# Optimization experiments

Measured on AMD Instinct MI355X. Metric: run time of the kernel, lower is better.

Reference implementation:

```python
import jax, jax.numpy as jnp
import numpy as np

N_NODES = 100000
N_EDGES = 1600000
IN_CH = 128
OUT_CH = 128


def setup_inputs() -> dict:
    key = jax.random.key(0)
    k1, k2, k3 = jax.random.split(key, 3)
    x = jax.random.normal(k1, (N_NODES, IN_CH), dtype=jnp.float32)
    edge_index = jax.random.randint(k2, (2, N_EDGES), 0, N_NODES, dtype=jnp.int64)
    # glorot-like init for the linear weight, stored as [in, out]
    W = jax.random.normal(k3, (IN_CH, OUT_CH), dtype=jnp.float32) * (2.0 / (IN_CH + OUT_CH)) ** 0.5
    bias = jnp.zeros((OUT_CH,), dtype=jnp.float32)
    return {"x": x, "edge_index": edge_index, "W": W, "bias": bias}


def reference(x, edge_index, W, bias):
    N = x.shape[0]
    # linear transform (bias-free, matches Linear(in, out, bias=False))
    h = x @ W  # [N, out]

    # add self loops (improved=False -> fill_value = 1.0)
    loop = jnp.arange(N, dtype=edge_index.dtype)
    src = jnp.concatenate([edge_index[0], loop])
    dst = jnp.concatenate([edge_index[1], loop])
    ew = jnp.ones(src.shape[0], dtype=h.dtype)  # edge_weight None -> ones

    # symmetric GCN normalization: deg from dst, norm = d^-1/2[src] * w * d^-1/2[dst]
    deg = jax.ops.segment_sum(ew, dst, num_segments=N)
    deg_inv_sqrt = jnp.where(deg > 0, jax.lax.rsqrt(deg), 0.0)
    w = deg_inv_sqrt[src] * ew * deg_inv_sqrt[dst]

    # spmm aggregation: out[dst] += w * h[src]
    out = jax.ops.segment_sum(h[src] * w[:, None], dst, num_segments=N)
    return out + bias
```

## Files before the change

### kernel.cpp

```cpp
#include <hip/hip_runtime.h>
#include <hip/hip_bf16.h>

constexpr int kNodes = 100000;
constexpr int kEdges = 1600000;
constexpr int kCh    = 128;
constexpr int kCap   = 32;
constexpr int kOvfCap = 8192;
constexpr int kPartSize = kNodes / 8;
constexpr int kCntStride = 32;
constexpr int kFillBlocks = 512;
constexpr int kGemmBlocks = (kNodes + 127) / 128;

typedef __attribute__((ext_vector_type(8))) short short8;
typedef __attribute__((ext_vector_type(4))) float floatx4;
typedef __attribute__((ext_vector_type(4))) int   intx4;


__global__ __launch_bounds__(512) void k_fused(const float* __restrict__ x,
                                               const float* __restrict__ W,
                                               const int* __restrict__ srcArr,
                                               const int* __restrict__ dstArr,
                                               int* __restrict__ cntPad,
                                               int* __restrict__ bucket,
                                               int* __restrict__ ovfCnt,
                                               int* __restrict__ ovfD,
                                               int* __restrict__ ovfS,
                                               __hip_bfloat16* __restrict__ hs) {
  if (blockIdx.x < kFillBlocks) {
    int part = blockIdx.x & 7;
    int bip  = blockIdx.x >> 3;
    int lo = part * kPartSize;
    const intx4* d4 = (const intx4*)dstArr;
    const intx4* s4 = (const intx4*)srcArr;
    for (int i = bip * 512 + (int)threadIdx.x; i < kEdges / 4; i += (kFillBlocks >> 3) * 512) {
      intx4 dv = __builtin_nontemporal_load(d4 + i);
      intx4 sv = __builtin_nontemporal_load(s4 + i);
      #pragma unroll
      for (int k = 0; k < 4; k++) {
        int d = dv[k];
        if ((unsigned)(d - lo) < (unsigned)kPartSize) {
          int pos = atomicAdd(&cntPad[(long)d * kCntStride], 1);
          if (pos < kCap) {
            bucket[(long)d * kCap + pos] = sv[k];
          } else {
            int o = atomicAdd(ovfCnt, 1);
            if (o < kOvfCap) { ovfD[o] = d; ovfS[o] = sv[k]; }
          }
        }
      }
    }
    return;
  }

  __shared__ short8 Bf[2048];
  for (int e = threadIdx.x; e < 2048; e += 512) {
    int lane = e & 63, c = (e >> 6) & 3, tt = e >> 8;
    int quad = lane >> 4, mcol = lane & 15;
    short8 v;
    #pragma unroll
    for (int j = 0; j < 8; j++) {
      __hip_bfloat16 h = __float2bfloat16(W[(c * 32 + quad * 8 + j) * kCh + tt * 16 + mcol]);
      v[j] = *(short*)&h;
    }
    Bf[e] = v;
  }
  __syncthreads();

  int wave = threadIdx.x >> 6;
  int lane = threadIdx.x & 63;
  int quad = lane >> 4;
  int mcol = lane & 15;
  int gb = blockIdx.x - kFillBlocks;
  long rowBase = ((long)gb * 8 + wave) * 16;
  if (rowBase >= kNodes) return;

  long arow = rowBase + mcol;
  if (arow >= kNodes) arow = kNodes - 1;
  const float* xp = x + arow * kCh;
  short8 afrag[4];
  #pragma unroll
  for (int c = 0; c < 4; c++) {
    const floatx4* p = (const floatx4*)(xp + c * 32 + quad * 8);
    floatx4 v0 = __builtin_nontemporal_load(p);
    floatx4 v1 = __builtin_nontemporal_load(p + 1);
    #pragma unroll
    for (int j = 0; j < 4; j++) {
      __hip_bfloat16 h0 = __float2bfloat16(v0[j]);
      __hip_bfloat16 h1 = __float2bfloat16(v1[j]);
      afrag[c][j]     = *(short*)&h0;
      afrag[c][j + 4] = *(short*)&h1;
    }
  }

  #pragma unroll
  for (int t = 0; t < 8; t++) {
    floatx4 acc = {0.f, 0.f, 0.f, 0.f};
    #pragma unroll
    for (int c = 0; c < 4; c++) {
      short8 b = Bf[(t * 4 + c) * 64 + lane];
      acc = __builtin_amdgcn_mfma_f32_16x16x32_bf16(afrag[c], b, acc, 0, 0, 0);
    }
    #pragma unroll
    for (int i = 0; i < 4; i++) {
      long r = rowBase + quad * 4 + i;
      if (r < kNodes) {
        __hip_bfloat16 h = __float2bfloat16(acc[i]);
        __builtin_nontemporal_store(*(short*)&h, (short*)hs + r * kCh + t * 16 + mcol);
      }
    }
  }
}


__global__ __launch_bounds__(256) void k_dinv(const int* __restrict__ cntPad,
                                              int* __restrict__ cntC,
                                              float* __restrict__ dinv) {
  int i = blockIdx.x * 256 + threadIdx.x;
  if (i < kNodes) {
    int c = cntPad[(long)i * kCntStride];
    cntC[i] = c;
    dinv[i] = rsqrtf((float)(c + 1));
  }
}


__global__ __launch_bounds__(256) void k_aggregate(const int* __restrict__ cntC,
                                                   const int* __restrict__ bucket,
                                                   const float* __restrict__ dinv,
                                                   const int* __restrict__ ovfCnt,
                                                   const int* __restrict__ ovfD,
                                                   const int* __restrict__ ovfS,
                                                   const __hip_bfloat16* __restrict__ hs,
                                                   const float* __restrict__ bias,
                                                   float* __restrict__ out) {
  int gid  = blockIdx.x * 256 + threadIdx.x;
  int node = gid >> 6;
  int lane = gid & 63;
  if (node >= kNodes) return;

  const __hip_bfloat162* hbase = (const __hip_bfloat162*)hs;

  int degRaw = cntC[node];
  float dd = dinv[node];

  float2 sf = __bfloat1622float2(hbase[(long)node * (kCh / 2) + lane]);
  float acc0 = dd * sf.x;
  float acc1 = dd * sf.y;

  int c = degRaw < kCap ? degRaw : kCap;
  const int* bkt = bucket + (long)node * kCap;

  int j = 0;
  for (; j + 7 < c; j += 8) {
    int s[8];
    #pragma unroll
    for (int u = 0; u < 8; u++) s[u] = bkt[j + u];
    float dv[8];
    #pragma unroll
    for (int u = 0; u < 8; u++) dv[u] = dinv[s[u]];
    __hip_bfloat162 v[8];
    #pragma unroll
    for (int u = 0; u < 8; u++) v[u] = hbase[(long)s[u] * (kCh / 2) + lane];
    #pragma unroll
    for (int u = 0; u < 8; u++) {
      float2 f = __bfloat1622float2(v[u]);
      acc0 = fmaf(dv[u], f.x, acc0);
      acc1 = fmaf(dv[u], f.y, acc1);
    }
  }
  for (; j < c; ++j) {
    int s = bkt[j];
    float dv = dinv[s];
    float2 f = __bfloat1622float2(hbase[(long)s * (kCh / 2) + lane]);
    acc0 = fmaf(dv, f.x, acc0);
    acc1 = fmaf(dv, f.y, acc1);
  }

  if (degRaw > kCap) {
    int n = *ovfCnt;
    if (n > kOvfCap) n = kOvfCap;
    for (int i = 0; i < n; i++) {
      if (ovfD[i] == node) {
        int s = ovfS[i];
        float2 f = __bfloat1622float2(hbase[(long)s * (kCh / 2) + lane]);
        acc0 = fmaf(dinv[s], f.x, acc0);
        acc1 = fmaf(dinv[s], f.y, acc1);
      }
    }
  }

  float2 b = ((const float2*)bias)[lane];
  float2 o;
  o.x = dd * acc0 + b.x;
  o.y = dd * acc1 + b.y;
  ((float2*)(out + (long)node * kCh))[lane] = o;
}


extern "C" void kernel_launch(void* const* d_in, const int* in_sizes, int n_in,
                              void* d_out, int out_size, void* d_ws, size_t ws_size,
                              hipStream_t stream) {
  const float* x    = (const float*)d_in[0];
  const int*   ei   = (const int*)d_in[1];
  const float* W    = (const float*)d_in[2];
  const float* bias = (const float*)d_in[3];
  float* out = (float*)d_out;

  const int* srcArr = ei;
  const int* dstArr = ei + kEdges;

  char* ws = (char*)d_ws;
  size_t off = 0;
  __hip_bfloat16* hs = (__hip_bfloat16*)(ws + off); off += (size_t)kNodes * kCh * 2;
  int*   bucket  = (int*)  (ws + off); off += (size_t)kNodes * kCap * 4;
  float* dinv    = (float*)(ws + off); off += (size_t)kNodes * 4;
  int*   cntC    = (int*)  (ws + off); off += (size_t)kNodes * 4;
  char* zbase = ws + off;
  int*   cntPad  = (int*)  (ws + off); off += (size_t)kNodes * kCntStride * 4;
  int*   ovfCnt  = (int*)  (ws + off); off += 128;
  size_t zbytes = (size_t)((ws + off) - zbase);
  int*   ovfD    = (int*)(ws + off); off += (size_t)kOvfCap * 4;
  int*   ovfS    = (int*)(ws + off); off += (size_t)kOvfCap * 4;

  (void)hipMemsetAsync(zbase, 0, zbytes, stream);

  k_fused<<<kFillBlocks + kGemmBlocks, 512, 0, stream>>>(x, W, srcArr, dstArr, cntPad, bucket,
                                                         ovfCnt, ovfD, ovfS, hs);

  k_dinv<<<(kNodes + 255) / 256, 256, 0, stream>>>(cntPad, cntC, dinv);

  long aggThreads = (long)kNodes * 64;
  int gAgg = (int)((aggThreads + 255) / 256);
  k_aggregate<<<gAgg, 256, 0, stream>>>(cntC, bucket, dinv, ovfCnt, ovfD, ovfS,
                                        hs, bias, out);
}
```

Before: 272.4 us.

## Replace global-atomic bucket fill with two-pass LDS binning of edges

The edge bucketing now runs in two passes. In the first, 128 blocks bin edges by destination range into per-block, per-bin chunks, packing dst offset and src into one word and counting with LDS atomics. In the second, a new fill kernel gathers each bin's chunks, builds the per-node buckets in shared memory, writes them out coalesced, and computes dinv. This replaces the scattered global atomics on padded counters and the separate dinv kernel. The cost is an extra intermediate buffer, chunk-overflow handling through a global flag that sends every node into the overflow scan, and a serial loop over 128 chunks per fill block.

After: 303.0 us. +11.2%, slower.

```diff
diff --git a/kernel.cpp b/kernel.cpp
--- a/kernel.cpp
+++ b/kernel.cpp
@@ -5,11 +5,15 @@
 constexpr int kEdges = 1600000;
 constexpr int kCh    = 128;
 constexpr int kCap   = 32;
-constexpr int kOvfCap = 8192;
-constexpr int kPartSize = kNodes / 8;
-constexpr int kCntStride = 32;
-constexpr int kFillBlocks = 512;
+constexpr int kOvfCap = 4096;
+constexpr int kBinShift = 11;
+constexpr int kBinSize  = 1 << kBinShift;
+constexpr int kBins  = (kNodes + kBinSize - 1) >> kBinShift;
+constexpr int kBinBlocks = 128;
+constexpr int kChunkCap = 384;
 constexpr int kGemmBlocks = (kNodes + 127) / 128;
+constexpr int kNodesPerB = 512;
+constexpr int kFillBlocks = (kNodes + kNodesPerB - 1) / kNodesPerB;
 
 typedef __attribute__((ext_vector_type(8))) short short8;
 typedef __attribute__((ext_vector_type(4))) float floatx4;
@@ -20,34 +24,43 @@
                                                const float* __restrict__ W,
                                                const int* __restrict__ srcArr,
                                                const int* __restrict__ dstArr,
-                                               int* __restrict__ cntPad,
-                                               int* __restrict__ bucket,
+                                               unsigned* __restrict__ segs,
+                                               int* __restrict__ segCnt,
+                                               int* __restrict__ cntA,
                                                int* __restrict__ ovfCnt,
+                                               int* __restrict__ ovfAFlag,
                                                int* __restrict__ ovfD,
                                                int* __restrict__ ovfS,
                                                __hip_bfloat16* __restrict__ hs) {
-  if (blockIdx.x < kFillBlocks) {
-    int part = blockIdx.x & 7;
-    int bip  = blockIdx.x >> 3;
-    int lo = part * kPartSize;
+  __shared__ int lcnt[kBins];
+  if (blockIdx.x < kBinBlocks) {
+    for (int i = threadIdx.x; i < kBins; i += 512) lcnt[i] = 0;
+    __syncthreads();
     const intx4* d4 = (const intx4*)dstArr;
     const intx4* s4 = (const intx4*)srcArr;
-    for (int i = bip * 512 + (int)threadIdx.x; i < kEdges / 4; i += (kFillBlocks >> 3) * 512) {
+    unsigned* myseg = segs + (long)blockIdx.x * kBins * kChunkCap;
+    for (int i = blockIdx.x * 512 + (int)threadIdx.x; i < kEdges / 4; i += kBinBlocks * 512) {
       intx4 dv = __builtin_nontemporal_load(d4 + i);
       intx4 sv = __builtin_nontemporal_load(s4 + i);
       #pragma unroll
       for (int k = 0; k < 4; k++) {
-        int d = dv[k];
-        if ((unsigned)(d - lo) < (unsigned)kPartSize) {
-          int pos = atomicAdd(&cntPad[(long)d * kCntStride], 1);
-          if (pos < kCap) {
-            bucket[(long)d * kCap + pos] = sv[k];
-          } else {
-            int o = atomicAdd(ovfCnt, 1);
-            if (o < kOvfCap) { ovfD[o] = d; ovfS[o] = sv[k]; }
-          }
+        int d = dv[k], s = sv[k];
+        int bin = d >> kBinShift;
+        int pos = atomicAdd(&lcnt[bin], 1);
+        if (pos < kChunkCap) {
+          myseg[bin * kChunkCap + pos] = ((unsigned)(d & (kBinSize - 1)) << 17) | (unsigned)s;
+        } else {
+          int o = atomicAdd(ovfCnt, 1);
+          if (o < kOvfCap) { ovfD[o] = d; ovfS[o] = s; }
+          atomicAdd(&cntA[d], 1);
+          atomicAdd(ovfAFlag, 1);
         }
       }
+    }
+    __syncthreads();
+    for (int i = threadIdx.x; i < kBins; i += 512) {
+      int c = lcnt[i];
+      segCnt[blockIdx.x * kBins + i] = c < kChunkCap ? c : kChunkCap;
     }
     return;
   }
@@ -70,7 +83,7 @@
   int lane = threadIdx.x & 63;
   int quad = lane >> 4;
   int mcol = lane & 15;
-  int gb = blockIdx.x - kFillBlocks;
+  int gb = blockIdx.x - kBinBlocks;
   long rowBase = ((long)gb * 8 + wave) * 16;
   if (rowBase >= kNodes) return;
 
@@ -112,14 +125,61 @@
 }
 
 
-__global__ __launch_bounds__(256) void k_dinv(const int* __restrict__ cntPad,
+__global__ __launch_bounds__(256) void k_fill(const unsigned* __restrict__ segs,
+                                              const int* __restrict__ segCnt,
+                                              const int* __restrict__ cntA,
                                               int* __restrict__ cntC,
-                                              float* __restrict__ dinv) {
-  int i = blockIdx.x * 256 + threadIdx.x;
-  if (i < kNodes) {
-    int c = cntPad[(long)i * kCntStride];
-    cntC[i] = c;
-    dinv[i] = rsqrtf((float)(c + 1));
+                                              float* __restrict__ dinv,
+                                              int* __restrict__ bucket,
+                                              int* __restrict__ ovfCnt,
+                                              int* __restrict__ ovfD,
+                                              int* __restrict__ ovfS) {
+  __shared__ int lsn[kBinBlocks];
+  __shared__ int lcnt[kNodesPerB];
+  __shared__ __align__(16) int lbkt[kNodesPerB][kCap];
+
+  int b   = blockIdx.x;
+  int lo  = b * kNodesPerB;
+  int bin = lo >> kBinShift;
+  int binBase = bin << kBinShift;
+  int sub = lo - binBase;
+
+  for (int i = threadIdx.x; i < kBinBlocks; i += 256) lsn[i] = segCnt[i * kBins + bin];
+  for (int i = threadIdx.x; i < kNodesPerB; i += 256) lcnt[i] = 0;
+  __syncthreads();
+
+  for (int blk = 0; blk < kBinBlocks; blk++) {
+    int n = lsn[blk];
+    const unsigned* chunk = segs + ((long)blk * kBins + bin) * kChunkCap;
+    for (int i = threadIdx.x; i < n; i += 256) {
+      unsigned e = chunk[i];
+      int r = (int)(e >> 17) - sub;
+      if ((unsigned)r < (unsigned)kNodesPerB) {
+        int pos = atomicAdd(&lcnt[r], 1);
+        if (pos < kCap) {
+          lbkt[r][pos] = (int)(e & 0x1ffff);
+        } else {
+          int o = atomicAdd(ovfCnt, 1);
+          if (o < kOvfCap) { ovfD[o] = binBase + sub + r; ovfS[o] = (int)(e & 0x1ffff); }
+        }
+      }
+    }
+  }
+  __syncthreads();
+
+  int hi = lo + kNodesPerB; if (hi > kNodes) hi = kNodes;
+  int nr = hi - lo;
+  for (int idx = threadIdx.x; idx < nr * (kCap / 4); idx += 256) {
+    int r = idx >> 3;
+    int q = idx & 7;
+    intx4 v = *((const intx4*)&lbkt[r][0] + q);
+    __builtin_nontemporal_store(v, (intx4*)(bucket + (long)(lo + r) * kCap) + q);
+  }
+  for (int r = threadIdx.x; r < nr; r += 256) {
+    int c = lcnt[r];
+    cntC[lo + r] = c;
+    int t = c + cntA[lo + r];
+    dinv[lo + r] = rsqrtf((float)(t + 1));
   }
 }
 
@@ -128,6 +188,7 @@
                                                    const int* __restrict__ bucket,
                                                    const float* __restrict__ dinv,
                                                    const int* __restrict__ ovfCnt,
+                                                   const int* __restrict__ ovfAFlag,
                                                    const int* __restrict__ ovfD,
                                                    const int* __restrict__ ovfS,
                                                    const __hip_bfloat16* __restrict__ hs,
@@ -176,7 +237,7 @@
     acc1 = fmaf(dv, f.y, acc1);
   }
 
-  if (degRaw > kCap) {
+  if (degRaw > kCap || *ovfAFlag != 0) {
     int n = *ovfCnt;
     if (n > kOvfCap) n = kOvfCap;
     for (int i = 0; i < n; i++) {
@@ -212,25 +273,30 @@
   char* ws = (char*)d_ws;
   size_t off = 0;
   __hip_bfloat16* hs = (__hip_bfloat16*)(ws + off); off += (size_t)kNodes * kCh * 2;
-  int*   bucket  = (int*)  (ws + off); off += (size_t)kNodes * kCap * 4;
-  float* dinv    = (float*)(ws + off); off += (size_t)kNodes * 4;
-  int*   cntC    = (int*)  (ws + off); off += (size_t)kNodes * 4;
+  int*   bucket  = (int*)     (ws + off); off += (size_t)kNodes * kCap * 4;
+  unsigned* segs = (unsigned*)(ws + off); off += (size_t)kBinBlocks * kBins * kChunkCap * 4;
+  float* dinv    = (float*)   (ws + off); off += (size_t)kNodes * 4;
+  int*   cntC    = (int*)     (ws + off); off += (size_t)kNodes * 4;
   char* zbase = ws + off;
-  int*   cntPad  = (int*)  (ws + off); off += (size_t)kNodes * kCntStride * 4;
-  int*   ovfCnt  = (int*)  (ws + off); off += 128;
+  int*   cntA    = (int*)(ws + off); off += (size_t)kNodes * 4;
+  int*   segCnt  = (int*)(ws + off); off += (size_t)kBinBlocks * kBins * 4;
+  int*   ovfCnt  = (int*)(ws + off); off += 64;
+  int*   ovfAFlag= (int*)(ws + off); off += 64;
   size_t zbytes = (size_t)((ws + off) - zbase);
   int*   ovfD    = (int*)(ws + off); off += (size_t)kOvfCap * 4;
   int*   ovfS    = (int*)(ws + off); off += (size_t)kOvfCap * 4;
 
   (void)hipMemsetAsync(zbase, 0, zbytes, stream);
 
-  k_fused<<<kFillBlocks + kGemmBlocks, 512, 0, stream>>>(x, W, srcArr, dstArr, cntPad, bucket,
-                                                         ovfCnt, ovfD, ovfS, hs);
-
-  k_dinv<<<(kNodes + 255) / 256, 256, 0, stream>>>(cntPad, cntC, dinv);
+  k_fused<<<kBinBlocks + kGemmBlocks, 512, 0, stream>>>(x, W, srcArr, dstArr,
+                                                        segs, segCnt, cntA,
+                                                        ovfCnt, ovfAFlag, ovfD, ovfS, hs);
+
+  k_fill<<<kFillBlocks, 256, 0, stream>>>(segs, segCnt, cntA, cntC, dinv, bucket,
+                                          ovfCnt, ovfD, ovfS);
 
   long aggThreads = (long)kNodes * 64;
   int gAgg = (int)((aggThreads + 255) / 256);
-  k_aggregate<<<gAgg, 256, 0, stream>>>(cntC, bucket, dinv, ovfCnt, ovfD, ovfS,
+  k_aggregate<<<gAgg, 256, 0, stream>>>(cntC, bucket, dinv, ovfCnt, ovfAFlag, ovfD, ovfS,
                                         hs, bias, out);
 }
```
